# Optimization experiments

Measured on AMD Instinct MI355X. Metric: run time of the kernel, lower is better.

The kernel has to match this reference:

```python
import jax, jax.numpy as jnp
import numpy as np
from jax import lax

BS, CI, NI, HI, WI = 16, 32, 8, 20, 20
CO, NO = 32, 8
ITERATIONS = 3


def setup_inputs() -> dict:
    key = jax.random.key(0)
    k1, k2 = jax.random.split(key)
    x = jax.random.normal(k1, (BS, CI, NI, HI, WI), dtype=jnp.float32)
    # conv weight: out_channels = co*no = 256, in_channels = ni = 8, 3x3
    W = jax.random.normal(k2, (CO * NO, NI, 3, 3), dtype=jnp.float32) * 0.05
    bias = jnp.zeros((CO, NO, 1, 1), dtype=jnp.float32)
    return {"x": x, "W": W, "bias": bias}


def squash(s, axis):
    # v = (|s|^2 / (1+|s|^2)) * s / |s|
    n2 = jnp.sum(s * s, axis=axis, keepdims=True)
    return s * (n2 / ((1.0 + n2) * jnp.sqrt(n2 + 1e-9)))


def reference(x, W, bias):
    bs, ci, ni, hi, wi = x.shape
    xr = x.reshape(bs * ci, ni, hi, wi)
    # conv2d, stride 1, padding 1, no bias
    votes = lax.conv_general_dilated(
        xr, W, window_strides=(1, 1), padding=[(1, 1), (1, 1)],
        dimension_numbers=("NCHW", "OIHW", "NCHW"))
    ho, wo = votes.shape[-2:]
    votes = votes.reshape(bs, ci, CO, NO, ho, wo)  # (bs,ci,co,no,ho,wo)
    logits = jnp.zeros((bs, ci, CO, ho, wo), dtype=votes.dtype)
    activation = None
    for _ in range(ITERATIONS):
        route = jax.nn.softmax(logits, axis=2)               # (bs,ci,co,ho,wo)
        # weighted sum of votes over input capsules ci, plus bias
        preact = jnp.sum(route[:, :, :, None] * votes, axis=1) + bias  # (bs,co,no,ho,wo)
        activation = squash(preact, axis=2)
        # agreement: dot over output atoms no
        distances = jnp.sum(votes * activation[:, None], axis=3)  # (bs,ci,co,ho,wo)
        logits = logits + distances
    return activation
```

## Files before the change

kernel.cpp:

```cpp
#include <hip/hip_runtime.h>

#define HH 20
#define WW 20

typedef _Float16 f16x8 __attribute__((ext_vector_type(8)));
typedef float    f32x4  __attribute__((ext_vector_type(4)));
typedef float    f32x4u __attribute__((ext_vector_type(4), aligned(4)));

template<int CTRL>
static __device__ __forceinline__ float dppf(float x) {
    return __int_as_float(__builtin_amdgcn_update_dpp(
        0, __float_as_int(x), CTRL, 0xF, 0xF, true));
}
static __device__ __forceinline__ float sum8_dpp(float x) {
    x += dppf<0xB1>(x);
    x += dppf<0x4E>(x);
    x += dppf<0x141>(x);
    return x;
}
static __device__ __forceinline__ float max8_dpp(float x) {
    x = fmaxf(x, dppf<0xB1>(x));
    x = fmaxf(x, dppf<0x4E>(x));
    x = fmaxf(x, dppf<0x141>(x));
    return x;
}

static __device__ __forceinline__ float bfly8_dpp(const float v[8], int lane) {
    const bool c1 = ((lane ^ (lane >> 2)) & 1);
    const bool c2 = (((lane >> 1) ^ (lane >> 2)) & 1);
    const bool c3 = ((lane >> 2) & 1);
    float k0 = c1 ? v[1] : v[0], s0 = c1 ? v[0] : v[1];
    float k1 = c1 ? v[3] : v[2], s1 = c1 ? v[2] : v[3];
    float k2 = c1 ? v[4] : v[5], s2 = c1 ? v[5] : v[4];
    float k3 = c1 ? v[6] : v[7], s3 = c1 ? v[7] : v[6];
    float w0 = k0 + dppf<0xB1>(s0);
    float w1 = k1 + dppf<0xB1>(s1);
    float w2 = k2 + dppf<0xB1>(s2);
    float w3 = k3 + dppf<0xB1>(s3);
    float ka = c2 ? w1 : w0, sa = c2 ? w0 : w1;
    float kb = c2 ? w2 : w3, sb = c2 ? w3 : w2;
    float za = ka + dppf<0x4E>(sa);
    float zb = kb + dppf<0x4E>(sb);
    float kr = c3 ? zb : za, sr = c3 ? za : zb;
    return kr + dppf<0x141>(sr);
}

__global__ void prepack_w_kernel(const float* __restrict__ Wt, _Float16* __restrict__ bp) {
    int idx = blockIdx.x * 256 + threadIdx.x;
    int oc = idx / 96, k = idx % 96;
    int r = k >> 3, ni = k & 7;
    float v = (r < 9) ? Wt[oc * 72 + ni * 9 + r] : 0.f;
    bp[idx] = (_Float16)v;
}

template<int DS>
__device__ __forceinline__ void stage_seg(const float* __restrict__ x,
                                          _Float16* A,
                                          int b, int h, int w0, int t) {
#pragma unroll
    for (int s = t; s < 768; s += 256) {
        int ci = s / 24;
        int r  = s % 24;
        int ni = r / 3, hr = r % 3;
        int hh = h - 1 + hr;
        bool hok = (hh >= 0) && (hh < HH);
        const int wlo = (DS == 0) ? (w0 - 1) : (DS < 0 ? 0 : WW - 4);
        const float* rowp = x + ((((b * 32 + ci) * 8 + ni) * HH + (hok ? hh : 0)) * WW) + wlo;
        f32x4u f4 = *(const f32x4u*)rowp;
        float vals[4];
        if (DS == 0)      { vals[0] = f4.x; vals[1] = f4.y; vals[2] = f4.z; vals[3] = f4.w; }
        else if (DS < 0)  { vals[0] = 0.f;  vals[1] = f4.x; vals[2] = f4.y; vals[3] = f4.z; }
        else              { vals[0] = f4.y; vals[1] = f4.z; vals[2] = f4.w; vals[3] = 0.f; }
        int kb = hr * 24 + ni;
#pragma unroll
        for (int j = 0; j < 4; ++j) {
            float v = hok ? vals[j] : 0.f;
            _Float16 hv = (_Float16)v;
            if (j < 3)  A[ci * 96 + kb + j * 8] = hv;
            if (j > 0)  A[(32 + ci) * 96 + kb + (j - 1) * 8] = hv;
        }
    }
}

__global__ __launch_bounds__(256, 4)
void caps_mfma11_kernel(const float* __restrict__ x,
                        const _Float16* __restrict__ bp,
                        const float* __restrict__ bias,
                        float* __restrict__ out) {
    __shared__ __align__(16) unsigned char region[18688];
    _Float16* A    = (_Float16*)region;
    float* bufbase = (float*)region;

    const int t  = threadIdx.x;
    const int wv = t >> 6;
    const int lr = t & 15;
    const int lg = (t >> 4) & 3;

    const int bi  = blockIdx.x;
    const int b   = bi / 200;
    const int rem = bi % 200;
    const int h   = rem / 10;
    const int w0  = (rem % 10) * 2;

#pragma unroll
    for (int e = t; e < 768; e += 256) {
        int row = e / 12, j = e % 12;
        ((unsigned int*)(A + row * 96 + 72))[j] = 0u;
    }

    const int dshift = (w0 == 0) ? -1 : (w0 == WW - 2) ? 1 : 0;
    if (dshift == 0)      stage_seg<0>(x, A, b, h, w0, t);
    else if (dshift < 0)  stage_seg<-1>(x, A, b, h, w0, t);
    else                  stage_seg<1>(x, A, b, h, w0, t);
    __syncthreads();

    f32x4 acc[4][4];
#pragma unroll
    for (int i = 0; i < 4; ++i)
#pragma unroll
        for (int mt = 0; mt < 4; ++mt) acc[i][mt] = (f32x4){0.f, 0.f, 0.f, 0.f};

#pragma unroll
    for (int kst = 0; kst < 3; ++kst) {
        const int kb = kst * 32 + lg * 8;
        f16x8 af0 = *(const f16x8*)&A[(lr)      * 96 + kb];
        f16x8 af1 = *(const f16x8*)&A[(16 + lr) * 96 + kb];
        f16x8 af2 = *(const f16x8*)&A[(32 + lr) * 96 + kb];
        f16x8 af3 = *(const f16x8*)&A[(48 + lr) * 96 + kb];
#pragma unroll
        for (int i = 0; i < 4; ++i) {
            const int oc = (wv * 4 + i) * 16 + lr;
            f16x8 bv = *(const f16x8*)&bp[oc * 96 + kb];
            acc[i][0] = __builtin_amdgcn_mfma_f32_16x16x32_f16(af0, bv, acc[i][0], 0, 0, 0);
            acc[i][1] = __builtin_amdgcn_mfma_f32_16x16x32_f16(af1, bv, acc[i][1], 0, 0, 0);
            acc[i][2] = __builtin_amdgcn_mfma_f32_16x16x32_f16(af2, bv, acc[i][2], 0, 0, 0);
            acc[i][3] = __builtin_amdgcn_mfma_f32_16x16x32_f16(af3, bv, acc[i][3], 0, 0, 0);
        }
    }
    __syncthreads();

    float* buf = bufbase + wv * 1152;
    f32x4 vr[2][4][2];
    const int ch_t = (t >> 5) & 1;
    const int c8   = t & 24;

#pragma unroll
    for (int p = 0; p < 2; ++p) {
#pragma unroll
        for (int ch = 0; ch < 2; ++ch) {
#pragma unroll
            for (int ii = 0; ii < 2; ++ii) {
#pragma unroll
                for (int mm = 0; mm < 2; ++mm) {
#pragma unroll
                    for (int r = 0; r < 4; ++r)
                        buf[(mm * 16 + lg * 4 + r) * 36 + ii * 16 + lr] =
                            acc[ch * 2 + ii][p * 2 + mm][r];
                }
            }
            if (ch_t == ch) {
#pragma unroll
                for (int q = 0; q < 4; ++q) {
                    int ciq = (t & 7) * 4 + q;
                    vr[p][q][0] = *(const f32x4*)&buf[ciq * 36 + c8];
                    vr[p][q][1] = *(const f32x4*)&buf[ciq * 36 + c8 + 4];
                }
            }
        }
    }

    const int co = t >> 3;
    const int no = t & 7;
    const float bsv = bias[t];
    float* route0 = bufbase;
    float* route1 = bufbase + 1152;
    float (*lg0)[37] = (float (*)[37])(bufbase + 2304);
    float (*lg1)[37] = (float (*)[37])(bufbase + 2304 + 1184);
    float dlog[2][4];
    float act[2];
    const int lbase = t & 56;

#pragma unroll
    for (int px = 0; px < 2; ++px) {
        float pj[8];
#pragma unroll
        for (int j = 0; j < 4; ++j) {
            pj[j]     = vr[px][0][0][j] + vr[px][1][0][j] + vr[px][2][0][j] + vr[px][3][0][j];
            pj[4 + j] = vr[px][0][1][j] + vr[px][1][1][j] + vr[px][2][1][j] + vr[px][3][1][j];
        }
        float p = fmaf(bfly8_dpp(pj, t), 0.03125f, bsv);
        float n2 = sum8_dpp(p * p);
        act[px] = p * n2 * __builtin_amdgcn_rcpf(1.f + n2) * __builtin_amdgcn_rsqf(n2 + 1e-9f);

        float a[8];
#pragma unroll
        for (int j = 0; j < 8; ++j) a[j] = __shfl(act[px], lbase | j);
#pragma unroll
        for (int q = 0; q < 4; ++q) {
            f32x4 v0 = vr[px][q][0], v1 = vr[px][q][1];
            dlog[px][q] = v0.x * a[0] + v0.y * a[1] + v0.z * a[2] + v0.w * a[3]
                        + v1.x * a[4] + v1.y * a[5] + v1.z * a[6] + v1.w * a[7];
        }
    }
    __syncthreads();
#pragma unroll
    for (int px = 0; px < 2; ++px) {
        float (*lgp)[37] = px ? lg1 : lg0;
#pragma unroll
        for (int q = 0; q < 4; ++q) lgp[no * 4 + q][co] = dlog[px][q];
    }
    __syncthreads();

#pragma unroll
    for (int it = 1; it < 3; ++it) {
#pragma unroll
        for (int px = 0; px < 2; ++px) {
            float (*lgp)[37] = px ? lg1 : lg0;
            float* rtp = px ? route1 : route0;
            float l0 = lgp[co][no],      l1 = lgp[co][no + 8];
            float l2 = lgp[co][no + 16], l3 = lgp[co][no + 24];
            float m = max8_dpp(fmaxf(fmaxf(l0, l1), fmaxf(l2, l3)));
            float e0 = __expf(l0 - m), e1 = __expf(l1 - m);
            float e2 = __expf(l2 - m), e3 = __expf(l3 - m);
            float s = sum8_dpp(e0 + e1 + e2 + e3);
            float inv = __builtin_amdgcn_rcpf(s);
            rtp[(no)      * 36 + co] = e0 * inv;
            rtp[(no + 8)  * 36 + co] = e1 * inv;
            rtp[(no + 16) * 36 + co] = e2 * inv;
            rtp[(no + 24) * 36 + co] = e3 * inv;
        }
        __syncthreads();

#pragma unroll
        for (int px = 0; px < 2; ++px) {
            float* rtp = px ? route1 : route0;
            f32x4 rv = *(const f32x4*)&rtp[co * 36 + (t & 7) * 4];
            float pj[8];
#pragma unroll
            for (int j = 0; j < 4; ++j) {
                pj[j]     = rv.x * vr[px][0][0][j] + rv.y * vr[px][1][0][j]
                          + rv.z * vr[px][2][0][j] + rv.w * vr[px][3][0][j];
                pj[4 + j] = rv.x * vr[px][0][1][j] + rv.y * vr[px][1][1][j]
                          + rv.z * vr[px][2][1][j] + rv.w * vr[px][3][1][j];
            }
            float p = bsv + bfly8_dpp(pj, t);
            float n2 = sum8_dpp(p * p);
            act[px] = p * n2 * __builtin_amdgcn_rcpf(1.f + n2) * __builtin_amdgcn_rsqf(n2 + 1e-9f);

            if (it == 1) {
                float a[8];
#pragma unroll
                for (int j = 0; j < 8; ++j) a[j] = __shfl(act[px], lbase | j);
                float (*lgp)[37] = px ? lg1 : lg0;
#pragma unroll
                for (int q = 0; q < 4; ++q) {
                    f32x4 v0 = vr[px][q][0], v1 = vr[px][q][1];
                    float d = v0.x * a[0] + v0.y * a[1] + v0.z * a[2] + v0.w * a[3]
                            + v1.x * a[4] + v1.y * a[5] + v1.z * a[6] + v1.w * a[7];
                    dlog[px][q] += d;
                    lgp[no * 4 + q][co] = dlog[px][q];
                }
            }
        }
        if (it == 1) __syncthreads();
    }

    float2 o2 = make_float2(act[0], act[1]);
    *(float2*)&out[(b * 256 + t) * 400 + h * 20 + w0] = o2;
}

extern "C" void kernel_launch(void* const* d_in, const int* in_sizes, int n_in,
                              void* d_out, int out_size, void* d_ws, size_t ws_size,
                              hipStream_t stream) {
    const float* x    = (const float*)d_in[0];
    const float* Wt   = (const float*)d_in[1];
    const float* bias = (const float*)d_in[2];
    float* out        = (float*)d_out;
    _Float16* bp      = (_Float16*)d_ws;

    prepack_w_kernel<<<dim3(96), dim3(256), 0, stream>>>(Wt, bp);
    caps_mfma11_kernel<<<dim3(3200), dim3(256), 0, stream>>>(x, bp, bias, out);
}
```

Measured before the change: 49.29 us.

## Pack fp16 staging writes as pairs and use LDS broadcast for activations

Staging now loads two adjacent ni rows per thread and writes a packed pair of fp16 values as 32-bit LDS stores, which halves the number of staging iterations and narrow LDS writes. The eight per-lane __shfl calls that broadcast activations are replaced by one LDS store plus two vector LDS reads. The logits are now written transposed as vectorized f32x4 stores, which removes one __syncthreads. LDS use grows from 18688 to 29696 bytes, which could limit occupancy at four blocks per CU.

```diff
diff --git a/kernel.cpp b/kernel.cpp
--- a/kernel.cpp
+++ b/kernel.cpp
@@ -24,7 +24,6 @@
     x = fmaxf(x, dppf<0x141>(x));
     return x;
 }
-
 static __device__ __forceinline__ float bfly8_dpp(const float v[8], int lane) {
     const bool c1 = ((lane ^ (lane >> 2)) & 1);
     const bool c2 = (((lane >> 1) ^ (lane >> 2)) & 1);
@@ -55,41 +54,47 @@
 
 template<int DS>
 __device__ __forceinline__ void stage_seg(const float* __restrict__ x,
-                                          _Float16* A,
+                                          unsigned* A32,
                                           int b, int h, int w0, int t) {
 #pragma unroll
-    for (int s = t; s < 768; s += 256) {
-        int ci = s / 24;
-        int r  = s % 24;
-        int ni = r / 3, hr = r % 3;
+    for (int s = t; s < 384; s += 256) {
+        int ci = s / 12;
+        int r  = s % 12;
+        int np = r / 3, hr = r % 3;
         int hh = h - 1 + hr;
         bool hok = (hh >= 0) && (hh < HH);
         const int wlo = (DS == 0) ? (w0 - 1) : (DS < 0 ? 0 : WW - 4);
-        const float* rowp = x + ((((b * 32 + ci) * 8 + ni) * HH + (hok ? hh : 0)) * WW) + wlo;
-        f32x4u f4 = *(const f32x4u*)rowp;
-        float vals[4];
-        if (DS == 0)      { vals[0] = f4.x; vals[1] = f4.y; vals[2] = f4.z; vals[3] = f4.w; }
-        else if (DS < 0)  { vals[0] = 0.f;  vals[1] = f4.x; vals[2] = f4.y; vals[3] = f4.z; }
-        else              { vals[0] = f4.y; vals[1] = f4.z; vals[2] = f4.w; vals[3] = 0.f; }
-        int kb = hr * 24 + ni;
+        const float* rowp = x + ((((b * 32 + ci) * 8 + 2 * np) * HH + (hok ? hh : 0)) * WW) + wlo;
+        f32x4u fa = *(const f32x4u*)rowp;
+        f32x4u fb = *(const f32x4u*)(rowp + HH * WW);
+        float va[4], vb[4];
+        if (DS == 0)      { va[0]=fa.x; va[1]=fa.y; va[2]=fa.z; va[3]=fa.w;
+                            vb[0]=fb.x; vb[1]=fb.y; vb[2]=fb.z; vb[3]=fb.w; }
+        else if (DS < 0)  { va[0]=0.f;  va[1]=fa.x; va[2]=fa.y; va[3]=fa.z;
+                            vb[0]=0.f;  vb[1]=fb.x; vb[2]=fb.y; vb[3]=fb.z; }
+        else              { va[0]=fa.y; va[1]=fa.z; va[2]=fa.w; va[3]=0.f;
+                            vb[0]=fb.y; vb[1]=fb.z; vb[2]=fb.w; vb[3]=0.f; }
 #pragma unroll
         for (int j = 0; j < 4; ++j) {
-            float v = hok ? vals[j] : 0.f;
-            _Float16 hv = (_Float16)v;
-            if (j < 3)  A[ci * 96 + kb + j * 8] = hv;
-            if (j > 0)  A[(32 + ci) * 96 + kb + (j - 1) * 8] = hv;
+            float v0 = hok ? va[j] : 0.f;
+            float v1 = hok ? vb[j] : 0.f;
+            unsigned short h0 = __builtin_bit_cast(unsigned short, (_Float16)v0);
+            unsigned short h1 = __builtin_bit_cast(unsigned short, (_Float16)v1);
+            unsigned pk = (unsigned)h0 | ((unsigned)h1 << 16);
+            if (j < 3)  A32[ci * 48 + (hr * 3 + j) * 4 + np] = pk;
+            if (j > 0)  A32[(32 + ci) * 48 + (hr * 3 + (j - 1)) * 4 + np] = pk;
         }
     }
 }
 
 __global__ __launch_bounds__(256, 4)
-void caps_mfma11_kernel(const float* __restrict__ x,
+void caps_mfma12_kernel(const float* __restrict__ x,
                         const _Float16* __restrict__ bp,
                         const float* __restrict__ bias,
                         float* __restrict__ out) {
-    __shared__ __align__(16) unsigned char region[18688];
-    _Float16* A    = (_Float16*)region;
-    float* bufbase = (float*)region;
+    __shared__ __align__(16) float Rf[7424];
+    _Float16* A    = (_Float16*)Rf;
+    unsigned* A32  = (unsigned*)Rf;
 
     const int t  = threadIdx.x;
     const int wv = t >> 6;
@@ -105,13 +110,13 @@
 #pragma unroll
     for (int e = t; e < 768; e += 256) {
         int row = e / 12, j = e % 12;
-        ((unsigned int*)(A + row * 96 + 72))[j] = 0u;
+        A32[row * 48 + 36 + j] = 0u;
     }
 
     const int dshift = (w0 == 0) ? -1 : (w0 == WW - 2) ? 1 : 0;
-    if (dshift == 0)      stage_seg<0>(x, A, b, h, w0, t);
-    else if (dshift < 0)  stage_seg<-1>(x, A, b, h, w0, t);
-    else                  stage_seg<1>(x, A, b, h, w0, t);
+    if (dshift == 0)      stage_seg<0>(x, A32, b, h, w0, t);
+    else if (dshift < 0)  stage_seg<-1>(x, A32, b, h, w0, t);
+    else                  stage_seg<1>(x, A32, b, h, w0, t);
     __syncthreads();
 
     f32x4 acc[4][4];
@@ -139,7 +144,7 @@
     }
     __syncthreads();
 
-    float* buf = bufbase + wv * 1152;
+    float* buf = Rf + wv * 1152;
     f32x4 vr[2][4][2];
     const int ch_t = (t >> 5) & 1;
     const int c8   = t & 24;
@@ -172,13 +177,14 @@
     const int co = t >> 3;
     const int no = t & 7;
     const float bsv = bias[t];
-    float* route0 = bufbase;
-    float* route1 = bufbase + 1152;
-    float (*lg0)[37] = (float (*)[37])(bufbase + 2304);
-    float (*lg1)[37] = (float (*)[37])(bufbase + 2304 + 1184);
+    float* route0 = Rf;
+    float* route1 = Rf + 1152;
+    float* lgT0   = Rf + 4608;
+    float* lgT1   = Rf + 5760;
+    float* actl   = Rf + 6912;
     float dlog[2][4];
     float act[2];
-    const int lbase = t & 56;
+    const int abase = wv * 128 + (t & 56);
 
 #pragma unroll
     for (int px = 0; px < 2; ++px) {
@@ -192,33 +198,34 @@
         float n2 = sum8_dpp(p * p);
         act[px] = p * n2 * __builtin_amdgcn_rcpf(1.f + n2) * __builtin_amdgcn_rsqf(n2 + 1e-9f);
 
-        float a[8];
-#pragma unroll
-        for (int j = 0; j < 8; ++j) a[j] = __shfl(act[px], lbase | j);
+        actl[wv * 128 + px * 64 + (t & 63)] = act[px];
+        f32x4 a0 = *(const f32x4*)&actl[abase + px * 64];
+        f32x4 a1 = *(const f32x4*)&actl[abase + px * 64 + 4];
+        float (*dst)[4] = &dlog[px];
+        f32x4 d4;
 #pragma unroll
         for (int q = 0; q < 4; ++q) {
             f32x4 v0 = vr[px][q][0], v1 = vr[px][q][1];
-            dlog[px][q] = v0.x * a[0] + v0.y * a[1] + v0.z * a[2] + v0.w * a[3]
-                        + v1.x * a[4] + v1.y * a[5] + v1.z * a[6] + v1.w * a[7];
-        }
+            float d = v0.x * a0.x + v0.y * a0.y + v0.z * a0.z + v0.w * a0.w
+                    + v1.x * a1.x + v1.y * a1.y + v1.z * a1.z + v1.w * a1.w;
+            (*dst)[q] = d;
+            d4[q] = d;
+        }
+        float* lgp = px ? lgT1 : lgT0;
+        *(f32x4*)&lgp[co * 36 + (t & 7) * 4] = d4;
     }
     __syncthreads();
-#pragma unroll
-    for (int px = 0; px < 2; ++px) {
-        float (*lgp)[37] = px ? lg1 : lg0;
-#pragma unroll
-        for (int q = 0; q < 4; ++q) lgp[no * 4 + q][co] = dlog[px][q];
-    }
-    __syncthreads();
 
 #pragma unroll
     for (int it = 1; it < 3; ++it) {
 #pragma unroll
         for (int px = 0; px < 2; ++px) {
-            float (*lgp)[37] = px ? lg1 : lg0;
+            float* lgp = px ? lgT1 : lgT0;
             float* rtp = px ? route1 : route0;
-            float l0 = lgp[co][no],      l1 = lgp[co][no + 8];
-            float l2 = lgp[co][no + 16], l3 = lgp[co][no + 24];
+            float l0 = lgp[(no)      * 36 + co];
+            float l1 = lgp[(no + 8)  * 36 + co];
+            float l2 = lgp[(no + 16) * 36 + co];
+            float l3 = lgp[(no + 24) * 36 + co];
             float m = max8_dpp(fmaxf(fmaxf(l0, l1), fmaxf(l2, l3)));
             float e0 = __expf(l0 - m), e1 = __expf(l1 - m);
             float e2 = __expf(l2 - m), e3 = __expf(l3 - m);
@@ -248,18 +255,21 @@
             act[px] = p * n2 * __builtin_amdgcn_rcpf(1.f + n2) * __builtin_amdgcn_rsqf(n2 + 1e-9f);
 
             if (it == 1) {
-                float a[8];
-#pragma unroll
-                for (int j = 0; j < 8; ++j) a[j] = __shfl(act[px], lbase | j);
-                float (*lgp)[37] = px ? lg1 : lg0;
+                actl[wv * 128 + px * 64 + (t & 63)] = act[px];
+                f32x4 a0 = *(const f32x4*)&actl[abase + px * 64];
+                f32x4 a1 = *(const f32x4*)&actl[abase + px * 64 + 4];
+                float* lgp = px ? lgT1 : lgT0;
+                f32x4 d4;
 #pragma unroll
                 for (int q = 0; q < 4; ++q) {
                     f32x4 v0 = vr[px][q][0], v1 = vr[px][q][1];
-                    float d = v0.x * a[0] + v0.y * a[1] + v0.z * a[2] + v0.w * a[3]
-                            + v1.x * a[4] + v1.y * a[5] + v1.z * a[6] + v1.w * a[7];
-                    dlog[px][q] += d;
-                    lgp[no * 4 + q][co] = dlog[px][q];
+                    float d = v0.x * a0.x + v0.y * a0.y + v0.z * a0.z + v0.w * a0.w
+                            + v1.x * a1.x + v1.y * a1.y + v1.z * a1.z + v1.w * a1.w;
+                    d = dlog[px][q] + d;
+                    dlog[px][q] = d;
+                    d4[q] = d;
                 }
+                *(f32x4*)&lgp[co * 36 + (t & 7) * 4] = d4;
             }
         }
         if (it == 1) __syncthreads();
@@ -279,5 +289,5 @@
     _Float16* bp      = (_Float16*)d_ws;
 
     prepack_w_kernel<<<dim3(96), dim3(256), 0, stream>>>(Wt, bp);
-    caps_mfma11_kernel<<<dim3(3200), dim3(256), 0, stream>>>(x, bp, bias, out);
-}
+    caps_mfma12_kernel<<<dim3(3200), dim3(256), 0, stream>>>(x, bp, bias, out);
+}
```

New measurement: 67.17 us. +36.3%, slower.
